# Kernel tuning notes

Measured on AMD Instinct MI355X. Metric: run time of the kernel, lower is better.

## Reference

```python
import jax, jax.numpy as jnp
import numpy as np

INPUT_SIZE = 10
HIDDEN_SIZE = 20
T, B = 512, 4096


def setup_inputs() -> dict:
    key = jax.random.key(0)
    ks = jax.random.split(key, 7)
    # PyTorch LSTMCell init: uniform(-k, k), k = 1/sqrt(hidden_size)
    k = 1.0 / np.sqrt(HIDDEN_SIZE)
    u = lambda kk, shape: jax.random.uniform(kk, shape, jnp.float32, -k, k)
    return {
        "input_sequence": jax.random.normal(ks[0], (T, B, INPUT_SIZE), jnp.float32),
        "initial_h": jax.random.normal(ks[1], (B, HIDDEN_SIZE), jnp.float32),
        "initial_c": jax.random.normal(ks[2], (B, HIDDEN_SIZE), jnp.float32),
        "W_ih": u(ks[3], (4 * HIDDEN_SIZE, INPUT_SIZE)),
        "W_hh": u(ks[4], (4 * HIDDEN_SIZE, HIDDEN_SIZE)),
        "b_ih": u(ks[5], (4 * HIDDEN_SIZE,)),
        "b_hh": u(ks[6], (4 * HIDDEN_SIZE,)),
    }


def _lstm_scan(input_sequence, initial_h, initial_c, W_ih, W_hh, b_ih, b_hh):
    H = initial_h.shape[-1]
    # Precompute input projections for all timesteps in one big GEMM:
    # [T, B, 4H] = [T, B, I] @ [I, 4H]
    x_proj = jnp.einsum("tbi,gi->tbg", input_sequence, W_ih) + b_ih + b_hh

    def step(carry, xg):
        h, c = carry
        gates = xg + h @ W_hh.T  # [B, 4H]
        i, f, g, o = jnp.split(gates, 4, axis=-1)  # PyTorch gate order i,f,g,o
        i = jax.nn.sigmoid(i)
        f = jax.nn.sigmoid(f)
        g = jnp.tanh(g)
        o = jax.nn.sigmoid(o)
        c_new = f * c + i * g
        h_new = o * jnp.tanh(c_new)
        return (h_new, c_new), h_new

    (h, c), outputs = jax.lax.scan(step, (initial_h, initial_c), x_proj)
    return outputs, h, c


def reference(input_sequence, initial_h, initial_c, W_ih, W_hh, b_ih, b_hh):
    return _lstm_scan(input_sequence, initial_h, initial_c, W_ih, W_hh, b_ih, b_hh)
```

## Files before the change

kernel.cpp:

```cpp
#include <hip/hip_runtime.h>


#define T_STEPS 512
#define BATCH   4096
#define ISZ     10
#define HSZ     20
#define WPB     4
#define NTHR    (WPB * 64)

typedef float v2f __attribute__((ext_vector_type(2)));
typedef float v4f __attribute__((ext_vector_type(4)));

__device__ __forceinline__ v2f fma2(v2f a, v2f b, v2f c) {
    return __builtin_elementwise_fma(a, b, c);
}

#if defined(__has_builtin)
#if __has_builtin(__builtin_amdgcn_exp2f)
#define FAST_EXP2(x) __builtin_amdgcn_exp2f(x)
#endif
#if __has_builtin(__builtin_amdgcn_rcpf)
#define FAST_RCP(x) __builtin_amdgcn_rcpf(x)
#endif
#endif
#ifndef FAST_EXP2
#define FAST_EXP2(x) exp2f(x)
#endif
#ifndef FAST_RCP
#define FAST_RCP(x) (1.0f/(x))
#endif

__device__ __forceinline__ float dpp_xor1(float v) {
    return __int_as_float(__builtin_amdgcn_update_dpp(
        0, __float_as_int(v), 0xB1, 0xF, 0xF, true));
}

#define HSYNC()                                                   \
    do {                                                          \
        __builtin_amdgcn_wave_barrier();                          \
        __builtin_amdgcn_fence(__ATOMIC_ACQ_REL, "wavefront");    \
        __builtin_amdgcn_wave_barrier();                          \
    } while (0)

__global__ __launch_bounds__(NTHR)
__attribute__((amdgpu_waves_per_eu(4, 4)))
void lstm_fused_kernel(
    const float* __restrict__ x,
    const float* __restrict__ h0,
    const float* __restrict__ c0,
    const float* __restrict__ Wih,
    const float* __restrict__ Whh,
    const float* __restrict__ bih,
    const float* __restrict__ bhh,
    float* __restrict__ out)
{
    __shared__ __align__(16) float hbuf[WPB][HSZ];

    const int tid  = threadIdx.x;
    const int wid  = tid >> 6;
    const int lane = tid & 63;
    const int s    = lane & 1;
    const int jraw = lane >> 1;
    const bool live = (jraw < HSZ);
    const int j    = live ? jraw : (jraw - HSZ);
    const int gb   = blockIdx.x * WPB + wid;
    const bool st  = live && (s == 0);

    const float B0 = s ? -2.8853900817779268f : -1.4426950408889634f;
    const float A0 = s ? 2.0f : 1.0f;
    const float C0 = s ? -1.0f : 0.0f;

    v2f wi[2][5], wh[2][10];
    float bias[2];
#pragma unroll
    for (int k = 0; k < 2; ++k) {
        const int row = (2 * s + k) * HSZ + j;
        const v2f* wip = (const v2f*)(Wih + row * ISZ);
        const v2f* whp = (const v2f*)(Whh + row * HSZ);
#pragma unroll
        for (int q = 0; q < 5; ++q)  wi[k][q] = wip[q];
#pragma unroll
        for (int q = 0; q < 10; ++q) wh[k][q] = whp[q];
        bias[k] = bih[row] + bhh[row];
    }

    float c = c0[(size_t)gb * HSZ + j];
    if (st) hbuf[wid][j] = h0[(size_t)gb * HSZ + j];
    HSYNC();

    const float* xrow = x + (size_t)gb * ISZ;
    float* outp = out + (size_t)gb * HSZ + j;

    v2f nxA[5], nxB[5];
    {
        const v2f* x0p = (const v2f*)(xrow);
        const v2f* x1p = (const v2f*)(xrow + (size_t)BATCH * ISZ);
#pragma unroll
        for (int q = 0; q < 5; ++q) { nxA[q] = x0p[q]; nxB[q] = x1p[q]; }
    }

    float hn = 0.0f;

#define STEP(NX, TI)                                                          \
    {                                                                         \
         \
        const v4f* hq = (const v4f*)(&hbuf[wid][0]);                          \
        v4f h4[5];                                                            \
        _Pragma("unroll")                                                     \
        for (int m = 0; m < 5; ++m) h4[m] = hq[m];                            \
                  \
        v2f a0 = {bias[0], 0.0f}, a1 = {bias[1], 0.0f};                       \
        _Pragma("unroll")                                                     \
        for (int q = 0; q < 5; ++q) {                                         \
            a0 = fma2(wi[0][q], NX[q], a0);                                   \
            a1 = fma2(wi[1][q], NX[q], a1);                                   \
        }                                                                     \
                     \
        {                                                                     \
            int tp = (TI) + 2; if (tp > T_STEPS - 1) tp = T_STEPS - 1;        \
            const v2f* xp = (const v2f*)(xrow + (size_t)tp * (BATCH * ISZ));  \
            _Pragma("unroll")                                                 \
            for (int q = 0; q < 5; ++q) NX[q] = xp[q];                        \
        }                                                                     \
                                                 \
        _Pragma("unroll")                                                     \
        for (int m = 0; m < 5; ++m) {                                         \
            const v2f lo = {h4[m].x, h4[m].y};                                \
            const v2f hi = {h4[m].z, h4[m].w};                                \
            a0 = fma2(wh[0][2 * m], lo, a0);                                  \
            a0 = fma2(wh[0][2 * m + 1], hi, a0);                              \
            a1 = fma2(wh[1][2 * m], lo, a1);                                  \
            a1 = fma2(wh[1][2 * m + 1], hi, a1);                              \
        }                                                                     \
        const float g0 = a0.x + a0.y;                                         \
        const float g1 = a1.x + a1.y;                                         \
           \
        const float act0 = A0 * FAST_RCP(1.0f + FAST_EXP2(g0 * B0)) + C0;     \
        const float act1 = FAST_RCP(1.0f +                                    \
                           FAST_EXP2(g1 * -1.4426950408889634f));             \
              \
        const float p0 = dpp_xor1(act0);                 \
        const float p1 = dpp_xor1(act1);                 \
                  \
        c = __builtin_fmaf(act1, c, act0 * p0);                               \
        const float th = 2.0f * FAST_RCP(1.0f +                               \
                         FAST_EXP2(c * -2.8853900817779268f)) - 1.0f;         \
        hn = p1 * th;                                                         \
        if (st) {                                                             \
            hbuf[wid][j] = hn;                  \
            outp[(size_t)(TI) * (BATCH * HSZ)] = hn;       \
        }                                                                     \
        HSYNC();          \
    }

    for (int t = 0; t < T_STEPS; t += 2) {
        STEP(nxA, t)
        STEP(nxB, t + 1)
    }
#undef STEP

    if (st) {
        const size_t tail = (size_t)T_STEPS * BATCH * HSZ;
        out[tail + (size_t)gb * HSZ + j] = hn;
        out[tail + (size_t)BATCH * HSZ + (size_t)gb * HSZ + j] = c;
    }
}

extern "C" void kernel_launch(void* const* d_in, const int* in_sizes, int n_in,
                              void* d_out, int out_size, void* d_ws, size_t ws_size,
                              hipStream_t stream) {
    const float* x   = (const float*)d_in[0];
    const float* h0  = (const float*)d_in[1];
    const float* c0  = (const float*)d_in[2];
    const float* Wih = (const float*)d_in[3];
    const float* Whh = (const float*)d_in[4];
    const float* bih = (const float*)d_in[5];
    const float* bhh = (const float*)d_in[6];
    float* out = (float*)d_out;

    const int nblk = BATCH / WPB;
    lstm_fused_kernel<<<nblk, NTHR, 0, stream>>>(x, h0, c0, Wih, Whh, bih, bhh, out);
}
```

Baseline: 498.8 us.

## Stage LSTM weights in LDS and reload per step to cut register pressure

Weights and combined biases move from per-thread registers into a padded shared-memory table (stride 36) that is re-read with vector LDS loads every timestep. This frees VGPRs, and the waves_per_eu(4,4) constraint is dropped. The per-step wave sync is reduced to a bare wave_barrier with no memory fence. The cost is extra LDS traffic on every step of the serial recurrence, and without the fence the write-then-read of the hidden-state buffer within a wave may not be ordered correctly.

```diff
diff --git a/kernel.cpp b/kernel.cpp
--- a/kernel.cpp
+++ b/kernel.cpp
@@ -7,13 +7,16 @@
 #define HSZ     20
 #define WPB     4
 #define NTHR    (WPB * 64)
+#define WSTR    36
 
 typedef float v2f __attribute__((ext_vector_type(2)));
 typedef float v4f __attribute__((ext_vector_type(4)));
 
-__device__ __forceinline__ v2f fma2(v2f a, v2f b, v2f c) {
+static __device__ __forceinline__ v2f fma2(v2f a, v2f b, v2f c) {
     return __builtin_elementwise_fma(a, b, c);
 }
+static __device__ __forceinline__ v2f vlo(v4f v) { return (v2f){v.x, v.y}; }
+static __device__ __forceinline__ v2f vhi(v4f v) { return (v2f){v.z, v.w}; }
 
 #if defined(__has_builtin)
 #if __has_builtin(__builtin_amdgcn_exp2f)
@@ -35,16 +38,7 @@
         0, __float_as_int(v), 0xB1, 0xF, 0xF, true));
 }
 
-#define HSYNC()                                                   \
-    do {                                                          \
-        __builtin_amdgcn_wave_barrier();                          \
-        __builtin_amdgcn_fence(__ATOMIC_ACQ_REL, "wavefront");    \
-        __builtin_amdgcn_wave_barrier();                          \
-    } while (0)
-
-__global__ __launch_bounds__(NTHR)
-__attribute__((amdgpu_waves_per_eu(4, 4)))
-void lstm_fused_kernel(
+__global__ __launch_bounds__(NTHR) void lstm_fused_kernel(
     const float* __restrict__ x,
     const float* __restrict__ h0,
     const float* __restrict__ c0,
@@ -54,9 +48,22 @@
     const float* __restrict__ bhh,
     float* __restrict__ out)
 {
+    __shared__ __align__(16) float wlds[80 * WSTR];
     __shared__ __align__(16) float hbuf[WPB][HSZ];
 
-    const int tid  = threadIdx.x;
+    const int tid = threadIdx.x;
+
+    for (int i = tid; i < 80 * ISZ; i += NTHR) {
+        const int row = i / ISZ, k = i - row * ISZ;
+        wlds[row * WSTR + k] = Wih[i];
+    }
+    for (int i = tid; i < 80 * HSZ; i += NTHR) {
+        const int row = i / HSZ, k = i - row * HSZ;
+        wlds[row * WSTR + 12 + k] = Whh[i];
+    }
+    for (int i = tid; i < 80; i += NTHR)
+        wlds[i * WSTR + 10] = bih[i] + bhh[i];
+
     const int wid  = tid >> 6;
     const int lane = tid & 63;
     const int s    = lane & 1;
@@ -66,27 +73,17 @@
     const int gb   = blockIdx.x * WPB + wid;
     const bool st  = live && (s == 0);
 
-    const float B0 = s ? -2.8853900817779268f : -1.4426950408889634f;
-    const float A0 = s ? 2.0f : 1.0f;
-    const float C0 = s ? -1.0f : 0.0f;
+    const float B0c = s ? -2.8853900817779268f : -1.4426950408889634f;
+    const float A0c = s ? 2.0f : 1.0f;
+    const float C0c = s ? -1.0f : 0.0f;
 
-    v2f wi[2][5], wh[2][10];
-    float bias[2];
-#pragma unroll
-    for (int k = 0; k < 2; ++k) {
-        const int row = (2 * s + k) * HSZ + j;
-        const v2f* wip = (const v2f*)(Wih + row * ISZ);
-        const v2f* whp = (const v2f*)(Whh + row * HSZ);
-#pragma unroll
-        for (int q = 0; q < 5; ++q)  wi[k][q] = wip[q];
-#pragma unroll
-        for (int q = 0; q < 10; ++q) wh[k][q] = whp[q];
-        bias[k] = bih[row] + bhh[row];
-    }
+    const float* wr0 = &wlds[((2 * s)     * HSZ + j) * WSTR];
+    const float* wr1 = &wlds[((2 * s + 1) * HSZ + j) * WSTR];
 
     float c = c0[(size_t)gb * HSZ + j];
     if (st) hbuf[wid][j] = h0[(size_t)gb * HSZ + j];
-    HSYNC();
+
+    __syncthreads();
 
     const float* xrow = x + (size_t)gb * ISZ;
     float* outp = out + (size_t)gb * HSZ + j;
@@ -103,18 +100,24 @@
 
 #define STEP(NX, TI)                                                          \
     {                                                                         \
-         \
+            \
+        const v4f* W0 = (const v4f*)wr0;                                      \
+        const v4f* W1 = (const v4f*)wr1;                                      \
+        v4f wq0[8], wq1[8];                                                   \
+        _Pragma("unroll")                                                     \
+        for (int m = 0; m < 8; ++m) { wq0[m] = W0[m]; wq1[m] = W1[m]; }       \
+                   \
         const v4f* hq = (const v4f*)(&hbuf[wid][0]);                          \
         v4f h4[5];                                                            \
         _Pragma("unroll")                                                     \
         for (int m = 0; m < 5; ++m) h4[m] = hq[m];                            \
-                  \
-        v2f a0 = {bias[0], 0.0f}, a1 = {bias[1], 0.0f};                       \
-        _Pragma("unroll")                                                     \
-        for (int q = 0; q < 5; ++q) {                                         \
-            a0 = fma2(wi[0][q], NX[q], a0);                                   \
-            a1 = fma2(wi[1][q], NX[q], a1);                                   \
-        }                                                                     \
+                                 \
+        v2f a0 = {wq0[2].z, 0.0f}, a1 = {wq1[2].z, 0.0f};                     \
+        a0 = fma2(vlo(wq0[0]), NX[0], a0); a1 = fma2(vlo(wq1[0]), NX[0], a1); \
+        a0 = fma2(vhi(wq0[0]), NX[1], a0); a1 = fma2(vhi(wq1[0]), NX[1], a1); \
+        a0 = fma2(vlo(wq0[1]), NX[2], a0); a1 = fma2(vlo(wq1[1]), NX[2], a1); \
+        a0 = fma2(vhi(wq0[1]), NX[3], a0); a1 = fma2(vhi(wq1[1]), NX[3], a1); \
+        a0 = fma2(vlo(wq0[2]), NX[4], a0); a1 = fma2(vlo(wq1[2]), NX[4], a1); \
                      \
         {                                                                     \
             int tp = (TI) + 2; if (tp > T_STEPS - 1) tp = T_STEPS - 1;        \
@@ -125,17 +128,15 @@
                                                  \
         _Pragma("unroll")                                                     \
         for (int m = 0; m < 5; ++m) {                                         \
-            const v2f lo = {h4[m].x, h4[m].y};                                \
-            const v2f hi = {h4[m].z, h4[m].w};                                \
-            a0 = fma2(wh[0][2 * m], lo, a0);                                  \
-            a0 = fma2(wh[0][2 * m + 1], hi, a0);                              \
-            a1 = fma2(wh[1][2 * m], lo, a1);                                  \
-            a1 = fma2(wh[1][2 * m + 1], hi, a1);                              \
+            a0 = fma2(vlo(wq0[3 + m]), vlo(h4[m]), a0);                       \
+            a0 = fma2(vhi(wq0[3 + m]), vhi(h4[m]), a0);                       \
+            a1 = fma2(vlo(wq1[3 + m]), vlo(h4[m]), a1);                       \
+            a1 = fma2(vhi(wq1[3 + m]), vhi(h4[m]), a1);                       \
         }                                                                     \
         const float g0 = a0.x + a0.y;                                         \
         const float g1 = a1.x + a1.y;                                         \
            \
-        const float act0 = A0 * FAST_RCP(1.0f + FAST_EXP2(g0 * B0)) + C0;     \
+        const float act0 = A0c * FAST_RCP(1.0f + FAST_EXP2(g0 * B0c)) + C0c;  \
         const float act1 = FAST_RCP(1.0f +                                    \
                            FAST_EXP2(g1 * -1.4426950408889634f));             \
               \
@@ -150,7 +151,7 @@
             hbuf[wid][j] = hn;                  \
             outp[(size_t)(TI) * (BATCH * HSZ)] = hn;       \
         }                                                                     \
-        HSYNC();          \
+        __builtin_amdgcn_wave_barrier();      \
     }
 
     for (int t = 0; t < T_STEPS; t += 2) {
```

Result: slower. 668.0 us (+33.9%).
